# Optimization experiments

Hardware: AMD Instinct MI355X
Metric: run time of the kernel (lower is better)

The kernel has to match this reference:

```python
import jax, jax.numpy as jnp
import numpy as np

E = 65536          # number of edges (cell pairs)
D = 256            # hidden_dim
P = 8              # n_lr_pairs


def setup_inputs() -> dict:
    key = jax.random.key(0)
    k1, k2, k3, k4, k5, k6, k7 = jax.random.split(key, 7)
    scale = 1.0 / np.sqrt(D)
    z_src = jax.random.normal(k1, (E, D), dtype=jnp.float32)
    z_dst = jax.random.normal(k2, (E, D), dtype=jnp.float32)
    lr_pair_idx = jax.random.randint(k3, (E,), 0, P, dtype=jnp.int64)
    # Per-LR-pair Linear(D, D): y = x @ W.T + b  (torch convention, W: [out, in])
    W_lr = jax.random.normal(k4, (P, D, D), dtype=jnp.float32) * scale
    b_lr = jax.random.normal(k5, (P, D), dtype=jnp.float32) * scale
    # nn.Bilinear(D, D, 1): weight [1, D, D], bias [1]
    W_bil = jax.random.normal(k6, (1, D, D), dtype=jnp.float32) * scale
    b_bil = jax.random.normal(k7, (1,), dtype=jnp.float32) * scale
    return {"z_src": z_src, "z_dst": z_dst, "W_lr": W_lr, "b_lr": b_lr,
            "W_bil": W_bil, "b_bil": b_bil, "lr_pair_idx": lr_pair_idx}


def _forward(z_src, z_dst, W_lr, b_lr, W_bil, b_bil, lr_pair_idx):
    # Per-LR-pair linear projection of z_src (MoE-style routing).
    # Fixed small loop over P experts; each iteration is a dense GEMM over
    # all E edges, masked to the edges routed to that pair. All idx values
    # lie in [0, P), so the zeros-init in the original is fully overwritten.
    z_proj = jnp.zeros_like(z_src)
    for p in range(P):
        mask = (lr_pair_idx == p)[:, None]                      # [E, 1]
        y_p = z_src @ W_lr[p].T + b_lr[p]                       # [E, D]
        z_proj = jnp.where(mask, y_p, z_proj)
    # Bilinear scoring: score_e = z_proj_e @ W_bil[0] @ z_dst_e + b_bil
    t = z_proj @ W_bil[0]                                       # [E, D]
    scores = jnp.sum(t * z_dst, axis=-1, keepdims=True) + b_bil  # [E, 1]
    return scores


def reference(z_src, z_dst, W_lr, b_lr, W_bil, b_bil, lr_pair_idx):
    return _forward(z_src, z_dst, W_lr, b_lr, W_bil, b_bil, lr_pair_idx)
```

## Files before the change

kernel.cpp:

```cpp
#include <hip/hip_runtime.h>
#include <hip/hip_bf16.h>
#include <cstddef>

#define NE 65536
#define ND 256
#define NP 8
#define RBLK 64
#define EPB (NE / RBLK)
#define TR 32
#define MAXT 2056

typedef short bf16x8 __attribute__((ext_vector_type(8)));
typedef float f32x4  __attribute__((ext_vector_type(4)));

__device__ __forceinline__ unsigned short f2bf(float f) {
  unsigned int u = __float_as_uint(f);
  u += 0x7FFFu + ((u >> 16) & 1u);
  return (unsigned short)(u >> 16);
}
__device__ __forceinline__ float bf2f(unsigned short h) {
  return __uint_as_float(((unsigned int)h) << 16);
}
__device__ __forceinline__ int load_idx(const void* idxraw, int is32, int e) {
  return is32 ? ((const int*)idxraw)[e] : (int)((const long long*)idxraw)[e];
}
__device__ __forceinline__ int sniff_is32(const void* idxraw, int* lflag, int bsel) {
  int tid = threadIdx.x;
  if (tid == 0) *lflag = 0;
  __syncthreads();
  const unsigned int* w = (const unsigned int*)idxraw;
  unsigned int val = w[((bsel & 63) * 256 + tid) * 2 + 1];
  if (__any(val != 0) && (tid & 63) == 0) atomicOr(lflag, 1);
  __syncthreads();
  return *lflag;
}

__global__ __launch_bounds__(256) void k_pre0(const float* __restrict__ Wbil,
                                              const float* __restrict__ blr,
                                              const void* __restrict__ idxraw,
                                              unsigned short* __restrict__ WbT,
                                              float* __restrict__ v,
                                              int* __restrict__ counts) {
  int b = blockIdx.x, t = threadIdx.x;
  if (b < 32) {
    int s = b * 256 + t;
    int kt = s >> 10, c = (s >> 6) & 15, l = s & 63;
    int col = c * 16 + (l & 15);
    int k0 = kt * 32 + (l >> 4) * 8;
    union { uint4 u; unsigned short h[8]; } uu;
#pragma unroll
    for (int j = 0; j < 8; ++j)
      uu.h[j] = f2bf(Wbil[(k0 + j) * ND + col]);
    *(uint4*)(WbT + (size_t)s * 8) = uu.u;
  } else if (b < 40) {
    int p = b - 32;
    float s = 0.f;
    for (int k = 0; k < ND; ++k)
      s = fmaf(blr[p * ND + k], Wbil[k * ND + t], s);
    v[p * ND + t] = s;
  } else {
    __shared__ int h[NP];
    __shared__ int lflag;
    int hb = b - 40;
    int is32 = sniff_is32(idxraw, &lflag, hb);
    if (t < NP) h[t] = 0;
    __syncthreads();
    int base = hb * EPB;
#pragma unroll
    for (int i = 0; i < EPB / 256; ++i) {
      int p = load_idx(idxraw, is32, base + t + i * 256);
      atomicAdd(&h[p], 1);
    }
    __syncthreads();
    if (t < NP) counts[hb * NP + t] = h[t];
  }
}

__global__ __launch_bounds__(64) void k_scan(const int* __restrict__ counts,
                                             int* __restrict__ hdr,
                                             int* __restrict__ bases) {
  __shared__ int cnt[NP];
  __shared__ int off[NP + 1];
  int q = threadIdx.x;
  if (q < NP) {
    int s = 0;
    for (int b = 0; b < RBLK; ++b) s += counts[b * NP + q];
    cnt[q] = s;
  }
  __syncthreads();
  if (q == 0) {
    int o = 0, tt = 0;
    for (int p = 0; p < NP; ++p) {
      off[p] = o; hdr[p] = o; hdr[9 + p] = tt;
      o += cnt[p];
      tt += (cnt[p] + TR - 1) / TR;
    }
    off[NP] = o; hdr[NP] = o; hdr[9 + NP] = tt;
  }
  __syncthreads();
  if (q < NP) {
    int run = off[q];
    for (int b = 0; b < RBLK; ++b) {
      bases[b * NP + q] = run;
      run += counts[b * NP + q];
    }
  }
}

__global__ __launch_bounds__(256) void k_sc2(const void* __restrict__ idxraw,
                                             const int* __restrict__ bases,
                                             int* __restrict__ perm,
                                             const float* __restrict__ Wlr,
                                             const unsigned short* __restrict__ WbT,
                                             unsigned short* __restrict__ Cst) {
  __shared__ unsigned short aF[2048 * 8];
  int b = blockIdx.x, tid = threadIdx.x;
  if (b < 64) {
    __shared__ int cur[NP];
    __shared__ int lflag;
    int is32 = sniff_is32(idxraw, &lflag, b);
    if (tid < NP) cur[tid] = bases[b * NP + tid];
    __syncthreads();
    int base = b * EPB;
#pragma unroll
    for (int i = 0; i < EPB / 256; ++i) {
      int e = base + tid + i * 256;
      int p = load_idx(idxraw, is32, e);
      int slot = atomicAdd(&cur[p], 1);
      perm[slot] = e;
    }
    return;
  }
  int blk = b - 64;
  int p = blk >> 2;
  int i0 = (blk & 3) * 64;
  const float* Wp = Wlr + (size_t)p * ND * ND;
#pragma unroll
  for (int it = 0; it < 8; ++it) {
    int s = tid + it * 256;
    int kt = s >> 8, r = (s >> 6) & 3, l = s & 63;
    int i = r * 16 + (l & 15);
    int k0 = kt * 32 + (l >> 4) * 8;
    union { uint4 u; unsigned short h[8]; } uu;
#pragma unroll
    for (int j = 0; j < 8; ++j)
      uu.h[j] = f2bf(Wp[(size_t)(k0 + j) * ND + i0 + i]);
    *(uint4*)(aF + (size_t)s * 8) = uu.u;
  }
  __syncthreads();
  int w = tid >> 6, l = tid & 63;
  f32x4 zero = {0.f, 0.f, 0.f, 0.f};
  f32x4 acc[16];
#pragma unroll
  for (int c = 0; c < 16; ++c) acc[c] = zero;
  for (int kt = 0; kt < 8; ++kt) {
    bf16x8 a = *(const bf16x8*)(aF + (size_t)((kt * 4 + w) * 64 + l) * 8);
#pragma unroll
    for (int c = 0; c < 16; ++c) {
      bf16x8 bb = *(const bf16x8*)(WbT + (size_t)((kt * 16 + c) * 64 + l) * 8);
      acc[c] = __builtin_amdgcn_mfma_f32_16x16x32_bf16(a, bb, acc[c], 0, 0, 0);
    }
  }
  unsigned short* Cp = Cst + (size_t)p * ND * ND;
#pragma unroll
  for (int c = 0; c < 16; ++c) {
#pragma unroll
    for (int q = 0; q < 4; ++q) {
      int i = i0 + w * 16 + ((l >> 4) * 4) + q;
      int j = c * 16 + (l & 15);
      int pos = ((i >> 5) * 16 + (j >> 4)) * 512 + (((i >> 3) & 3) * 16 + (j & 15)) * 8 + (i & 7);
      Cp[pos] = f2bf(acc[c][q]);
    }
  }
}

__global__ __launch_bounds__(512, 8) void k_main(const float* __restrict__ zsrc,
                                                 const float* __restrict__ zdst,
                                                 const int* __restrict__ perm,
                                                 const int* __restrict__ hdr,
                                                 const unsigned short* __restrict__ Cst,
                                                 const float* __restrict__ v,
                                                 const float* __restrict__ bbil,
                                                 float* __restrict__ out) {
  __shared__ unsigned short zs[8192];
  __shared__ unsigned short zd[8192];
  __shared__ float red[8][TR];
  __shared__ int eids[TR];
  __shared__ int shdr[18];
  int tid = threadIdx.x;
  if (tid < 18) shdr[tid] = hdr[tid];
  __syncthreads();
  int bid = blockIdx.x;
  if (bid >= shdr[9 + NP]) return;
  int p = 0;
  while (p < NP - 1 && bid >= shdr[9 + p + 1]) ++p;
  int t = bid - shdr[9 + p];
  int cnt = shdr[p + 1] - shdr[p];
  int ebase = shdr[p] + t * TR;
  int nrow = cnt - t * TR; if (nrow > TR) nrow = TR;
  if (tid < TR) eids[tid] = perm[ebase + (tid < nrow ? tid : nrow - 1)];
  __syncthreads();
  int w = tid >> 6, l = tid & 63;
  int hh = l >> 4, rr = l & 15;

  int kt0 = l >> 3, q0 = (l >> 1) & 3, par0 = l & 1;
#pragma unroll
  for (int i = 0; i < 4; ++i) {
    int row = w * 4 + i;
    int e = eids[row];
    float4 fs = *(const float4*)(zsrc + (size_t)e * ND + l * 4);
    float4 fd = *(const float4*)(zdst + (size_t)e * ND + l * 4);
    union { unsigned long long u; unsigned short h[4]; } us, ud;
    us.h[0] = f2bf(fs.x); us.h[1] = f2bf(fs.y); us.h[2] = f2bf(fs.z); us.h[3] = f2bf(fs.w);
    ud.h[0] = f2bf(fd.x); ud.h[1] = f2bf(fd.y); ud.h[2] = f2bf(fd.z); ud.h[3] = f2bf(fd.w);
    unsigned g = (unsigned)((kt0 * 2 + (row >> 4)) * 64 + (row & 15) + 16 * q0);
    g ^= ((g >> 6) & 7u) << 1;
    *(unsigned long long*)((char*)zs + g * 16 + par0 * 8) = us.u;
    *(unsigned long long*)((char*)zd + ((unsigned)(row * 512 + l * 8) ^ (((unsigned)row & 7u) << 5))) = ud.u;
  }
  __syncthreads();

  const unsigned short* Cp = Cst + (size_t)p * ND * ND;
  f32x4 zero = {0.f, 0.f, 0.f, 0.f};
  f32x4 acc[2][2];
#pragma unroll
  for (int sr = 0; sr < 2; ++sr)
#pragma unroll
    for (int cl = 0; cl < 2; ++cl) acc[sr][cl] = zero;
#pragma unroll
  for (int kt = 0; kt < 8; ++kt) {
    bf16x8 a[2];
#pragma unroll
    for (int sr = 0; sr < 2; ++sr) {
      unsigned g = (unsigned)((kt * 2 + sr) * 64 + l);
      g ^= ((g >> 6) & 7u) << 1;
      a[sr] = *(const bf16x8*)((const char*)zs + g * 16);
    }
#pragma unroll
    for (int cl = 0; cl < 2; ++cl) {
      bf16x8 bb = *(const bf16x8*)(Cp + (size_t)((kt * 16 + (w * 2 + cl)) * 64 + l) * 8);
#pragma unroll
      for (int sr = 0; sr < 2; ++sr)
        acc[sr][cl] = __builtin_amdgcn_mfma_f32_16x16x32_bf16(a[sr], bb, acc[sr][cl], 0, 0, 0);
    }
  }

  float vloc[2];
#pragma unroll
  for (int cl = 0; cl < 2; ++cl)
    vloc[cl] = v[p * ND + (w * 2 + cl) * 16 + rr];
#pragma unroll
  for (int sr = 0; sr < 2; ++sr) {
#pragma unroll
    for (int q = 0; q < 4; ++q) {
      int row = sr * 16 + hh * 4 + q;
      unsigned swz = ((unsigned)row & 7u) << 5;
      float sv = 0.f;
#pragma unroll
      for (int cl = 0; cl < 2; ++cl) {
        int col = (w * 2 + cl) * 16 + rr;
        unsigned byte = ((unsigned)(row * 512 + col * 2)) ^ swz;
        sv = fmaf(acc[sr][cl][q] + vloc[cl], bf2f(*(const unsigned short*)((const char*)zd + byte)), sv);
      }
      sv += __shfl_xor(sv, 1, 64);
      sv += __shfl_xor(sv, 2, 64);
      sv += __shfl_xor(sv, 4, 64);
      sv += __shfl_xor(sv, 8, 64);
      if (rr == 0) red[w][row] = sv;
    }
  }
  __syncthreads();
  if (tid < TR && tid < nrow) {
    float sc = bbil[0];
#pragma unroll
    for (int ww = 0; ww < 8; ++ww) sc += red[ww][tid];
    out[eids[tid]] = sc;
  }
}

extern "C" void kernel_launch(void* const* d_in, const int* in_sizes, int n_in,
                              void* d_out, int out_size, void* d_ws, size_t ws_size,
                              hipStream_t stream) {
  const float* zsrc = (const float*)d_in[0];
  const float* zdst = (const float*)d_in[1];
  const float* Wlr  = (const float*)d_in[2];
  const float* blr  = (const float*)d_in[3];
  const float* Wbil = (const float*)d_in[4];
  const float* bbil = (const float*)d_in[5];
  const void*  idx  = (const void*)d_in[6];
  float* out = (float*)d_out;

  char* ws = (char*)d_ws;
  int* hdr    = (int*)ws;
  int* counts = (int*)(ws + 4096);
  int* bases  = (int*)(ws + 8192);
  int* perm   = (int*)(ws + 16384);
  unsigned short* WbT = (unsigned short*)(ws + 16384 + (size_t)NE * 4);
  float* v = (float*)(ws + 16384 + (size_t)NE * 4 + 131072);
  unsigned short* Cst = (unsigned short*)(ws + 16384 + (size_t)NE * 4 + 131072 + 8192);

  k_pre0<<<104, 256, 0, stream>>>(Wbil, blr, idx, WbT, v, counts);
  k_scan<<<1, 64, 0, stream>>>(counts, hdr, bases);
  k_sc2<<<96, 256, 0, stream>>>(idx, bases, perm, Wlr, WbT, Cst);
  k_main<<<MAXT, 512, 0, stream>>>(zsrc, zdst, perm, hdr, Cst, v, bbil, out);
}
```

Measured before the change: 77.90 us.

## Repack z_src/z_dst into expert-sorted bf16 buffers before the main GEMM

Adds a repack kernel that loads each 32-edge block of z_src/z_dst into LDS, computes per-expert ranks with wave ballots, and writes bf16 rows into permuted, expert-contiguous workspace buffers. The main kernel then reads those rows contiguously instead of gathering fp32 rows through perm. Counting is rewritten to use ballots over 32-edge sub-blocks, with a wider scan, and the scatter is split from the W_lr x W_bil precompute. This adds a full extra read and write pass over both inputs plus more launches, in exchange for coalesced, half-width loads in the main kernel. A gather fallback path runs when the workspace is too small.

After: 110.5 us. +41.9%, slower.

```diff
diff --git a/kernel.cpp b/kernel.cpp
--- a/kernel.cpp
+++ b/kernel.cpp
@@ -5,13 +5,15 @@
 #define NE 65536
 #define ND 256
 #define NP 8
-#define RBLK 64
-#define EPB (NE / RBLK)
+#define SB 32
+#define NSB (NE / SB)
 #define TR 32
 #define MAXT 2056
 
 typedef short bf16x8 __attribute__((ext_vector_type(8)));
 typedef float f32x4  __attribute__((ext_vector_type(4)));
+typedef const __attribute__((address_space(1))) unsigned int* gas_t;
+typedef __attribute__((address_space(3))) unsigned int* las_t;
 
 __device__ __forceinline__ unsigned short f2bf(float f) {
   unsigned int u = __float_as_uint(f);
@@ -24,12 +26,12 @@
 __device__ __forceinline__ int load_idx(const void* idxraw, int is32, int e) {
   return is32 ? ((const int*)idxraw)[e] : (int)((const long long*)idxraw)[e];
 }
-__device__ __forceinline__ int sniff_is32(const void* idxraw, int* lflag, int bsel) {
+__device__ __forceinline__ int sniff_is32(const void* idxraw, int* lflag) {
   int tid = threadIdx.x;
   if (tid == 0) *lflag = 0;
   __syncthreads();
   const unsigned int* w = (const unsigned int*)idxraw;
-  unsigned int val = w[((bsel & 63) * 256 + tid) * 2 + 1];
+  unsigned int val = w[(((int)blockIdx.x & 63) * 256 + (tid & 255)) * 2 + 1];
   if (__any(val != 0) && (tid & 63) == 0) atomicOr(lflag, 1);
   __syncthreads();
   return *lflag;
@@ -59,81 +61,64 @@
       s = fmaf(blr[p * ND + k], Wbil[k * ND + t], s);
     v[p * ND + t] = s;
   } else {
-    __shared__ int h[NP];
     __shared__ int lflag;
+    int is32 = sniff_is32(idxraw, &lflag);
     int hb = b - 40;
-    int is32 = sniff_is32(idxraw, &lflag, hb);
-    if (t < NP) h[t] = 0;
-    __syncthreads();
-    int base = hb * EPB;
-#pragma unroll
-    for (int i = 0; i < EPB / 256; ++i) {
-      int p = load_idx(idxraw, is32, base + t + i * 256);
-      atomicAdd(&h[p], 1);
-    }
-    __syncthreads();
-    if (t < NP) counts[hb * NP + t] = h[t];
-  }
-}
-
-__global__ __launch_bounds__(64) void k_scan(const int* __restrict__ counts,
-                                             int* __restrict__ hdr,
-                                             int* __restrict__ bases) {
-  __shared__ int cnt[NP];
-  __shared__ int off[NP + 1];
-  int q = threadIdx.x;
-  if (q < NP) {
-    int s = 0;
-    for (int b = 0; b < RBLK; ++b) s += counts[b * NP + q];
-    cnt[q] = s;
-  }
-  __syncthreads();
-  if (q == 0) {
+    int w = t >> 6, l = t & 63;
+    int e = hb * 256 + w * 64 + l;
+    int p = load_idx(idxraw, is32, e);
+    int sb0 = hb * 8 + w * 2;
+#pragma unroll
+    for (int q = 0; q < NP; ++q) {
+      unsigned long long m = __ballot(p == q);
+      if (l == q)      counts[q * NSB + sb0]     = __popcll(m & 0xFFFFFFFFull);
+      if (l == 32 + q) counts[q * NSB + sb0 + 1] = __popcll(m >> 32);
+    }
+  }
+}
+
+__global__ __launch_bounds__(256) void k_scan(const int* __restrict__ counts,
+                                              int* __restrict__ hdr,
+                                              int* __restrict__ bases) {
+  __shared__ int part[NP][32], cpre[NP][32], cnt[NP], shoff[NP];
+  int t = threadIdx.x;
+  int q = t >> 5, i = t & 31;
+  int s = 0;
+  for (int j = 0; j < 64; ++j) s += counts[q * NSB + i * 64 + j];
+  part[q][i] = s;
+  __syncthreads();
+  if (t < NP) {
+    int run = 0;
+    for (int k = 0; k < 32; ++k) { cpre[t][k] = run; run += part[t][k]; }
+    cnt[t] = run;
+  }
+  __syncthreads();
+  if (t == 0) {
     int o = 0, tt = 0;
     for (int p = 0; p < NP; ++p) {
-      off[p] = o; hdr[p] = o; hdr[9 + p] = tt;
+      shoff[p] = o; hdr[p] = o; hdr[9 + p] = tt;
       o += cnt[p];
       tt += (cnt[p] + TR - 1) / TR;
     }
-    off[NP] = o; hdr[NP] = o; hdr[9 + NP] = tt;
-  }
-  __syncthreads();
-  if (q < NP) {
-    int run = off[q];
-    for (int b = 0; b < RBLK; ++b) {
-      bases[b * NP + q] = run;
-      run += counts[b * NP + q];
-    }
-  }
-}
-
-__global__ __launch_bounds__(256) void k_sc2(const void* __restrict__ idxraw,
-                                             const int* __restrict__ bases,
-                                             int* __restrict__ perm,
-                                             const float* __restrict__ Wlr,
-                                             const unsigned short* __restrict__ WbT,
-                                             unsigned short* __restrict__ Cst) {
+    hdr[NP] = o; hdr[9 + NP] = tt;
+  }
+  __syncthreads();
+  int run = shoff[q] + cpre[q][i];
+  for (int j = 0; j < 64; ++j) {
+    int sb = i * 64 + j;
+    bases[q * NSB + sb] = run;
+    run += counts[q * NSB + sb];
+  }
+}
+
+__global__ __launch_bounds__(256) void k_cpre(const float* __restrict__ Wlr,
+                                              const unsigned short* __restrict__ WbT,
+                                              unsigned short* __restrict__ Cst) {
   __shared__ unsigned short aF[2048 * 8];
-  int b = blockIdx.x, tid = threadIdx.x;
-  if (b < 64) {
-    __shared__ int cur[NP];
-    __shared__ int lflag;
-    int is32 = sniff_is32(idxraw, &lflag, b);
-    if (tid < NP) cur[tid] = bases[b * NP + tid];
-    __syncthreads();
-    int base = b * EPB;
-#pragma unroll
-    for (int i = 0; i < EPB / 256; ++i) {
-      int e = base + tid + i * 256;
-      int p = load_idx(idxraw, is32, e);
-      int slot = atomicAdd(&cur[p], 1);
-      perm[slot] = e;
-    }
-    return;
-  }
-  int blk = b - 64;
+  int blk = blockIdx.x;
   int p = blk >> 2;
   int i0 = (blk & 3) * 64;
+  int tid = threadIdx.x;
   const float* Wp = Wlr + (size_t)p * ND * ND;
 #pragma unroll
   for (int it = 0; it < 8; ++it) {
@@ -174,14 +159,95 @@
   }
 }
 
-__global__ __launch_bounds__(512, 8) void k_main(const float* __restrict__ zsrc,
-                                                 const float* __restrict__ zdst,
-                                                 const int* __restrict__ perm,
-                                                 const int* __restrict__ hdr,
-                                                 const unsigned short* __restrict__ Cst,
-                                                 const float* __restrict__ v,
-                                                 const float* __restrict__ bbil,
-                                                 float* __restrict__ out) {
+__global__ __launch_bounds__(256) void k_repack(const void* __restrict__ idxraw,
+                                                const float* __restrict__ zsrc,
+                                                const float* __restrict__ zdst,
+                                                const int* __restrict__ bases,
+                                                int* __restrict__ perm,
+                                                unsigned short* __restrict__ zsP,
+                                                unsigned short* __restrict__ zdP) {
+  __shared__ float zsL[SB * 256];
+  __shared__ float zdL[SB * 256];
+  __shared__ int lsrcS[SB], garowS[SB];
+  __shared__ int lflag;
+  int tid = threadIdx.x;
+  int b = blockIdx.x;
+  int is32 = sniff_is32(idxraw, &lflag);
+  int w = tid >> 6, l = tid & 63;
+  int base = b * SB;
+#pragma unroll
+  for (int i = 0; i < 16; ++i) {
+    int r = w * 16 + i;
+    const float* g = (r < SB) ? (zsrc + (size_t)(base + r) * ND + l * 4)
+                              : (zdst + (size_t)(base + r - SB) * ND + l * 4);
+    float* ldsb = (r < SB) ? (zsL + r * 256) : (zdL + (r - SB) * 256);
+    __builtin_amdgcn_global_load_lds((gas_t)(const void*)g,
+                                     (las_t)(void*)ldsb, 16, 0, 0);
+  }
+  if (w == 0) {
+    int p = (l < SB) ? load_idx(idxraw, is32, base + l) : 999;
+    unsigned long long lt = (l == 63) ? ~0ull >> 1 : ((1ull << l) - 1ull);
+    int loffq = 0, slot = 0, rank = 0, gq = 0;
+#pragma unroll
+    for (int q = 0; q < NP; ++q) {
+      unsigned long long m = __ballot(p == q);
+      if (p == q) { rank = __popcll(m & lt); slot = loffq + rank; gq = q; }
+      loffq += __popcll(m);
+    }
+    if (l < SB) {
+      lsrcS[slot] = l;
+      int g = bases[gq * NSB + b] + rank;
+      garowS[slot] = g;
+      perm[g] = base + l;
+    }
+  }
+  __syncthreads();
+  int hw = tid >> 5, ln = tid & 31;
+#pragma unroll
+  for (int i = 0; i < 8; ++i) {
+    int orow = hw * 8 + i;
+    int s = orow & (SB - 1);
+    int n = lsrcS[s];
+    size_t g = (size_t)garowS[s];
+    const float* srcRow = (orow < SB) ? (zsL + n * 256) : (zdL + n * 256);
+    unsigned short* dst = ((orow < SB) ? zsP : zdP) + g * 256 + ln * 8;
+    float4 a0 = *(const float4*)(srcRow + ln * 8);
+    float4 a1 = *(const float4*)(srcRow + ln * 8 + 4);
+    union { uint4 u; unsigned short h[8]; } o;
+    o.h[0] = f2bf(a0.x); o.h[1] = f2bf(a0.y); o.h[2] = f2bf(a0.z); o.h[3] = f2bf(a0.w);
+    o.h[4] = f2bf(a1.x); o.h[5] = f2bf(a1.y); o.h[6] = f2bf(a1.z); o.h[7] = f2bf(a1.w);
+    *(uint4*)dst = o.u;
+  }
+}
+
+__global__ __launch_bounds__(64) void k_perm(const void* __restrict__ idxraw,
+                                             const int* __restrict__ bases,
+                                             int* __restrict__ perm) {
+  __shared__ int lflag;
+  int l = threadIdx.x;
+  int b = blockIdx.x;
+  int is32 = sniff_is32(idxraw, &lflag);
+  int base = b * SB;
+  int p = (l < SB) ? load_idx(idxraw, is32, base + l) : 999;
+  unsigned long long lt = (l == 63) ? ~0ull >> 1 : ((1ull << l) - 1ull);
+  int loffq = 0, rank = 0, gq = -1;
+#pragma unroll
+  for (int q = 0; q < NP; ++q) {
+    unsigned long long m = __ballot(p == q);
+    if (p == q) { rank = __popcll(m & lt); gq = q; }
+    loffq += __popcll(m);
+  }
+  if (l < SB) perm[bases[gq * NSB + b] + rank] = base + l;
+}
+
+__global__ __launch_bounds__(512, 8) void k_main_s(const unsigned short* __restrict__ zsP,
+                                                   const unsigned short* __restrict__ zdP,
+                                                   const int* __restrict__ perm,
+                                                   const int* __restrict__ hdr,
+                                                   const unsigned short* __restrict__ Cst,
+                                                   const float* __restrict__ v,
+                                                   const float* __restrict__ bbil,
+                                                   float* __restrict__ out) {
   __shared__ unsigned short zs[8192];
   __shared__ unsigned short zd[8192];
   __shared__ float red[8][TR];
@@ -199,10 +265,105 @@
   int ebase = shdr[p] + t * TR;
   int nrow = cnt - t * TR; if (nrow > TR) nrow = TR;
   if (tid < TR) eids[tid] = perm[ebase + (tid < nrow ? tid : nrow - 1)];
-  __syncthreads();
   int w = tid >> 6, l = tid & 63;
+  int kt0 = l >> 3, q0 = (l >> 1) & 3, par0 = l & 1;
+#pragma unroll
+  for (int i = 0; i < 4; ++i) {
+    int row = w * 4 + i;
+    int grow = ebase + row; if (grow > NE - 1) grow = NE - 1;
+    unsigned long long us = *(const unsigned long long*)(zsP + (size_t)grow * 256 + l * 4);
+    unsigned long long ud = *(const unsigned long long*)(zdP + (size_t)grow * 256 + l * 4);
+    unsigned g = (unsigned)((kt0 * 2 + (row >> 4)) * 64 + (row & 15) + 16 * q0);
+    g ^= ((g >> 6) & 7u) << 1;
+    *(unsigned long long*)((char*)zs + g * 16 + par0 * 8) = us;
+    *(unsigned long long*)((char*)zd + ((unsigned)(row * 512 + l * 8) ^ (((unsigned)row & 7u) << 5))) = ud;
+  }
+  __syncthreads();
+  const unsigned short* Cp = Cst + (size_t)p * ND * ND;
+  f32x4 zero = {0.f, 0.f, 0.f, 0.f};
+  f32x4 acc[2][2];
+#pragma unroll
+  for (int sr = 0; sr < 2; ++sr)
+#pragma unroll
+    for (int cl = 0; cl < 2; ++cl) acc[sr][cl] = zero;
   int hh = l >> 4, rr = l & 15;
-
+#pragma unroll
+  for (int kt = 0; kt < 8; ++kt) {
+    bf16x8 a[2];
+#pragma unroll
+    for (int sr = 0; sr < 2; ++sr) {
+      unsigned g = (unsigned)((kt * 2 + sr) * 64 + l);
+      g ^= ((g >> 6) & 7u) << 1;
+      a[sr] = *(const bf16x8*)((const char*)zs + g * 16);
+    }
+#pragma unroll
+    for (int cl = 0; cl < 2; ++cl) {
+      bf16x8 bb = *(const bf16x8*)(Cp + (size_t)((kt * 16 + (w * 2 + cl)) * 64 + l) * 8);
+#pragma unroll
+      for (int sr = 0; sr < 2; ++sr)
+        acc[sr][cl] = __builtin_amdgcn_mfma_f32_16x16x32_bf16(a[sr], bb, acc[sr][cl], 0, 0, 0);
+    }
+  }
+  float vloc[2];
+#pragma unroll
+  for (int cl = 0; cl < 2; ++cl)
+    vloc[cl] = v[p * ND + (w * 2 + cl) * 16 + rr];
+#pragma unroll
+  for (int sr = 0; sr < 2; ++sr) {
+#pragma unroll
+    for (int q = 0; q < 4; ++q) {
+      int row = sr * 16 + hh * 4 + q;
+      unsigned swz = ((unsigned)row & 7u) << 5;
+      float sv = 0.f;
+#pragma unroll
+      for (int cl = 0; cl < 2; ++cl) {
+        int col = (w * 2 + cl) * 16 + rr;
+        unsigned byte = ((unsigned)(row * 512 + col * 2)) ^ swz;
+        sv = fmaf(acc[sr][cl][q] + vloc[cl], bf2f(*(const unsigned short*)((const char*)zd + byte)), sv);
+      }
+      sv += __shfl_xor(sv, 1, 64);
+      sv += __shfl_xor(sv, 2, 64);
+      sv += __shfl_xor(sv, 4, 64);
+      sv += __shfl_xor(sv, 8, 64);
+      if (rr == 0) red[w][row] = sv;
+    }
+  }
+  __syncthreads();
+  if (tid < TR && tid < nrow) {
+    float sc = bbil[0];
+#pragma unroll
+    for (int ww = 0; ww < 8; ++ww) sc += red[ww][tid];
+    out[eids[tid]] = sc;
+  }
+}
+
+__global__ __launch_bounds__(512, 8) void k_main_g(const float* __restrict__ zsrc,
+                                                   const float* __restrict__ zdst,
+                                                   const int* __restrict__ perm,
+                                                   const int* __restrict__ hdr,
+                                                   const unsigned short* __restrict__ Cst,
+                                                   const float* __restrict__ v,
+                                                   const float* __restrict__ bbil,
+                                                   float* __restrict__ out) {
+  __shared__ unsigned short zs[8192];
+  __shared__ unsigned short zd[8192];
+  __shared__ float red[8][TR];
+  __shared__ int eids[TR];
+  __shared__ int shdr[18];
+  int tid = threadIdx.x;
+  if (tid < 18) shdr[tid] = hdr[tid];
+  __syncthreads();
+  int bid = blockIdx.x;
+  if (bid >= shdr[9 + NP]) return;
+  int p = 0;
+  while (p < NP - 1 && bid >= shdr[9 + p + 1]) ++p;
+  int t = bid - shdr[9 + p];
+  int cnt = shdr[p + 1] - shdr[p];
+  int ebase = shdr[p] + t * TR;
+  int nrow = cnt - t * TR; if (nrow > TR) nrow = TR;
+  if (tid < TR) eids[tid] = perm[ebase + (tid < nrow ? tid : nrow - 1)];
+  __syncthreads();
+  int w = tid >> 6, l = tid & 63;
   int kt0 = l >> 3, q0 = (l >> 1) & 3, par0 = l & 1;
 #pragma unroll
   for (int i = 0; i < 4; ++i) {
@@ -219,7 +380,6 @@
     *(unsigned long long*)((char*)zd + ((unsigned)(row * 512 + l * 8) ^ (((unsigned)row & 7u) << 5))) = ud.u;
   }
   __syncthreads();
-
   const unsigned short* Cp = Cst + (size_t)p * ND * ND;
   f32x4 zero = {0.f, 0.f, 0.f, 0.f};
   f32x4 acc[2][2];
@@ -227,6 +387,7 @@
   for (int sr = 0; sr < 2; ++sr)
 #pragma unroll
     for (int cl = 0; cl < 2; ++cl) acc[sr][cl] = zero;
+  int hh = l >> 4, rr = l & 15;
 #pragma unroll
   for (int kt = 0; kt < 8; ++kt) {
     bf16x8 a[2];
@@ -244,7 +405,6 @@
         acc[sr][cl] = __builtin_amdgcn_mfma_f32_16x16x32_bf16(a[sr], bb, acc[sr][cl], 0, 0, 0);
     }
   }
-
   float vloc[2];
 #pragma unroll
   for (int cl = 0; cl < 2; ++cl)
@@ -293,14 +453,23 @@
   char* ws = (char*)d_ws;
   int* hdr    = (int*)ws;
   int* counts = (int*)(ws + 4096);
-  int* bases  = (int*)(ws + 8192);
-  int* perm   = (int*)(ws + 16384);
-  unsigned short* WbT = (unsigned short*)(ws + 16384 + (size_t)NE * 4);
-  float* v = (float*)(ws + 16384 + (size_t)NE * 4 + 131072);
-  unsigned short* Cst = (unsigned short*)(ws + 16384 + (size_t)NE * 4 + 131072 + 8192);
-
-  k_pre0<<<104, 256, 0, stream>>>(Wbil, blr, idx, WbT, v, counts);
-  k_scan<<<1, 64, 0, stream>>>(counts, hdr, bases);
-  k_sc2<<<96, 256, 0, stream>>>(idx, bases, perm, Wlr, WbT, Cst);
-  k_main<<<MAXT, 512, 0, stream>>>(zsrc, zdst, perm, hdr, Cst, v, bbil, out);
-}
+  int* bases  = (int*)(ws + 73728);
+  unsigned short* WbT = (unsigned short*)(ws + 139264);
+  float* v            = (float*)(ws + 270336);
+  unsigned short* Cst = (unsigned short*)(ws + 278528);
+  int* perm           = (int*)(ws + 1327104);
+  unsigned short* zsP = (unsigned short*)(ws + 2097152);
+  unsigned short* zdP = (unsigned short*)(ws + 2097152 + 33554432);
+  size_t need = 2097152 + 2ull * 33554432;
+
+  k_pre0<<<296, 256, 0, stream>>>(Wbil, blr, idx, WbT, v, counts);
+  k_scan<<<1, 256, 0, stream>>>(counts, hdr, bases);
+  k_cpre<<<32, 256, 0, stream>>>(Wlr, WbT, Cst);
+  if (ws_size >= need) {
+    k_repack<<<NSB, 256, 0, stream>>>(idx, zsrc, zdst, bases, perm, zsP, zdP);
+    k_main_s<<<MAXT, 512, 0, stream>>>(zsP, zdP, perm, hdr, Cst, v, bbil, out);
+  } else {
+    k_perm<<<NSB, 64, 0, stream>>>(idx, bases, perm);
+    k_main_g<<<MAXT, 512, 0, stream>>>(zsrc, zdst, perm, hdr, Cst, v, bbil, out);
+  }
+}
```

## Make routing histogram and permutation deterministic via ballots and interleave expert tiles

Applied to the files above, without the earlier changes.

The per-block shared-memory atomic histogram and atomic scatter are replaced with wave ballot/popcount counts over 32-edge sub-blocks, a wider parallel scan, and a separate rank-based permutation kernel. Edges are now placed deterministically in order. The permutation scatter is split out of the fused weight-precompute kernel, adding one more launch. k_main now launches a fixed 16384-block grid with expert-interleaved block mapping, so tiles of different experts run at the same time, but many blocks exit early. The intent is to remove LDS atomic contention and the serial scan work, in exchange for extra launch overhead and idle blocks.

New measurement: 87.48 us. 12.3% more time.

```diff
diff --git a/kernel.cpp b/kernel.cpp
--- a/kernel.cpp
+++ b/kernel.cpp
@@ -5,10 +5,9 @@
 #define NE 65536
 #define ND 256
 #define NP 8
-#define RBLK 64
-#define EPB (NE / RBLK)
+#define SB 32
+#define NSB (NE / SB)
 #define TR 32
-#define MAXT 2056
 
 typedef short bf16x8 __attribute__((ext_vector_type(8)));
 typedef float f32x4  __attribute__((ext_vector_type(4)));
@@ -24,12 +23,12 @@
 __device__ __forceinline__ int load_idx(const void* idxraw, int is32, int e) {
   return is32 ? ((const int*)idxraw)[e] : (int)((const long long*)idxraw)[e];
 }
-__device__ __forceinline__ int sniff_is32(const void* idxraw, int* lflag, int bsel) {
+__device__ __forceinline__ int sniff_is32(const void* idxraw, int* lflag) {
   int tid = threadIdx.x;
   if (tid == 0) *lflag = 0;
   __syncthreads();
   const unsigned int* w = (const unsigned int*)idxraw;
-  unsigned int val = w[((bsel & 63) * 256 + tid) * 2 + 1];
+  unsigned int val = w[(((int)blockIdx.x & 63) * 256 + (tid & 255)) * 2 + 1];
   if (__any(val != 0) && (tid & 63) == 0) atomicOr(lflag, 1);
   __syncthreads();
   return *lflag;
@@ -59,81 +58,64 @@
       s = fmaf(blr[p * ND + k], Wbil[k * ND + t], s);
     v[p * ND + t] = s;
   } else {
-    __shared__ int h[NP];
     __shared__ int lflag;
+    int is32 = sniff_is32(idxraw, &lflag);
     int hb = b - 40;
-    int is32 = sniff_is32(idxraw, &lflag, hb);
-    if (t < NP) h[t] = 0;
-    __syncthreads();
-    int base = hb * EPB;
-#pragma unroll
-    for (int i = 0; i < EPB / 256; ++i) {
-      int p = load_idx(idxraw, is32, base + t + i * 256);
-      atomicAdd(&h[p], 1);
-    }
-    __syncthreads();
-    if (t < NP) counts[hb * NP + t] = h[t];
-  }
-}
-
-__global__ __launch_bounds__(64) void k_scan(const int* __restrict__ counts,
-                                             int* __restrict__ hdr,
-                                             int* __restrict__ bases) {
-  __shared__ int cnt[NP];
-  __shared__ int off[NP + 1];
-  int q = threadIdx.x;
-  if (q < NP) {
-    int s = 0;
-    for (int b = 0; b < RBLK; ++b) s += counts[b * NP + q];
-    cnt[q] = s;
-  }
-  __syncthreads();
-  if (q == 0) {
+    int w = t >> 6, l = t & 63;
+    int e = hb * 256 + w * 64 + l;
+    int p = load_idx(idxraw, is32, e);
+    int sb0 = hb * 8 + w * 2;
+#pragma unroll
+    for (int q = 0; q < NP; ++q) {
+      unsigned long long m = __ballot(p == q);
+      if (l == q)      counts[q * NSB + sb0]     = __popcll(m & 0xFFFFFFFFull);
+      if (l == 32 + q) counts[q * NSB + sb0 + 1] = __popcll(m >> 32);
+    }
+  }
+}
+
+__global__ __launch_bounds__(256) void k_scan(const int* __restrict__ counts,
+                                              int* __restrict__ hdr,
+                                              int* __restrict__ bases) {
+  __shared__ int part[NP][32], cpre[NP][32], cnt[NP], shoff[NP];
+  int t = threadIdx.x;
+  int q = t >> 5, i = t & 31;
+  int s = 0;
+  for (int j = 0; j < 64; ++j) s += counts[q * NSB + i * 64 + j];
+  part[q][i] = s;
+  __syncthreads();
+  if (t < NP) {
+    int run = 0;
+    for (int k = 0; k < 32; ++k) { cpre[t][k] = run; run += part[t][k]; }
+    cnt[t] = run;
+  }
+  __syncthreads();
+  if (t == 0) {
     int o = 0, tt = 0;
     for (int p = 0; p < NP; ++p) {
-      off[p] = o; hdr[p] = o; hdr[9 + p] = tt;
+      shoff[p] = o; hdr[p] = o; hdr[9 + p] = tt;
       o += cnt[p];
       tt += (cnt[p] + TR - 1) / TR;
     }
-    off[NP] = o; hdr[NP] = o; hdr[9 + NP] = tt;
-  }
-  __syncthreads();
-  if (q < NP) {
-    int run = off[q];
-    for (int b = 0; b < RBLK; ++b) {
-      bases[b * NP + q] = run;
-      run += counts[b * NP + q];
-    }
-  }
-}
-
-__global__ __launch_bounds__(256) void k_sc2(const void* __restrict__ idxraw,
-                                             const int* __restrict__ bases,
-                                             int* __restrict__ perm,
-                                             const float* __restrict__ Wlr,
-                                             const unsigned short* __restrict__ WbT,
-                                             unsigned short* __restrict__ Cst) {
+    hdr[NP] = o; hdr[9 + NP] = tt;
+  }
+  __syncthreads();
+  int run = shoff[q] + cpre[q][i];
+  for (int j = 0; j < 64; ++j) {
+    int sb = i * 64 + j;
+    bases[q * NSB + sb] = run;
+    run += counts[q * NSB + sb];
+  }
+}
+
+__global__ __launch_bounds__(256) void k_cpre(const float* __restrict__ Wlr,
+                                              const unsigned short* __restrict__ WbT,
+                                              unsigned short* __restrict__ Cst) {
   __shared__ unsigned short aF[2048 * 8];
-  int b = blockIdx.x, tid = threadIdx.x;
-  if (b < 64) {
-    __shared__ int cur[NP];
-    __shared__ int lflag;
-    int is32 = sniff_is32(idxraw, &lflag, b);
-    if (tid < NP) cur[tid] = bases[b * NP + tid];
-    __syncthreads();
-    int base = b * EPB;
-#pragma unroll
-    for (int i = 0; i < EPB / 256; ++i) {
-      int e = base + tid + i * 256;
-      int p = load_idx(idxraw, is32, e);
-      int slot = atomicAdd(&cur[p], 1);
-      perm[slot] = e;
-    }
-    return;
-  }
-  int blk = b - 64;
+  int blk = blockIdx.x;
   int p = blk >> 2;
   int i0 = (blk & 3) * 64;
+  int tid = threadIdx.x;
   const float* Wp = Wlr + (size_t)p * ND * ND;
 #pragma unroll
   for (int it = 0; it < 8; ++it) {
@@ -172,6 +154,33 @@
       Cp[pos] = f2bf(acc[c][q]);
     }
   }
+}
+
+__global__ __launch_bounds__(64) void k_perm(const void* __restrict__ idxraw,
+                                             const int* __restrict__ bases,
+                                             int* __restrict__ perm) {
+  __shared__ int lflag;
+  int l = threadIdx.x;
+  int b = blockIdx.x;
+  if (l == 0) lflag = 0;
+  __syncthreads();
+  {
+    const unsigned int* w = (const unsigned int*)idxraw;
+    unsigned int val = w[((b & 63) * 64 + l) * 2 + 1];
+    if (__any(val != 0) && l == 0) atomicOr(&lflag, 1);
+  }
+  __syncthreads();
+  int is32 = lflag;
+  int base = b * SB;
+  int p = (l < SB) ? load_idx(idxraw, is32, base + l) : 999;
+  unsigned long long lt = (l == 63) ? (~0ull >> 1) : ((1ull << l) - 1ull);
+  int rank = 0, gq = 0;
+#pragma unroll
+  for (int q = 0; q < NP; ++q) {
+    unsigned long long m = __ballot(p == q);
+    if (p == q) { rank = __popcll(m & lt); gq = q; }
+  }
+  if (l < SB) perm[bases[gq * NSB + b] + rank] = base + l;
 }
 
 __global__ __launch_bounds__(512, 8) void k_main(const float* __restrict__ zsrc,
@@ -191,18 +200,16 @@
   if (tid < 18) shdr[tid] = hdr[tid];
   __syncthreads();
   int bid = blockIdx.x;
-  if (bid >= shdr[9 + NP]) return;
-  int p = 0;
-  while (p < NP - 1 && bid >= shdr[9 + p + 1]) ++p;
-  int t = bid - shdr[9 + p];
+  int g = bid >> 3, r = bid & 7;
+  int p = g & 7;
+  int t = ((g >> 3) << 3) + r;
   int cnt = shdr[p + 1] - shdr[p];
+  if (t * TR >= cnt) return;
   int ebase = shdr[p] + t * TR;
   int nrow = cnt - t * TR; if (nrow > TR) nrow = TR;
   if (tid < TR) eids[tid] = perm[ebase + (tid < nrow ? tid : nrow - 1)];
   __syncthreads();
   int w = tid >> 6, l = tid & 63;
-  int hh = l >> 4, rr = l & 15;
-
   int kt0 = l >> 3, q0 = (l >> 1) & 3, par0 = l & 1;
 #pragma unroll
   for (int i = 0; i < 4; ++i) {
@@ -213,13 +220,12 @@
     union { unsigned long long u; unsigned short h[4]; } us, ud;
     us.h[0] = f2bf(fs.x); us.h[1] = f2bf(fs.y); us.h[2] = f2bf(fs.z); us.h[3] = f2bf(fs.w);
     ud.h[0] = f2bf(fd.x); ud.h[1] = f2bf(fd.y); ud.h[2] = f2bf(fd.z); ud.h[3] = f2bf(fd.w);
-    unsigned g = (unsigned)((kt0 * 2 + (row >> 4)) * 64 + (row & 15) + 16 * q0);
-    g ^= ((g >> 6) & 7u) << 1;
-    *(unsigned long long*)((char*)zs + g * 16 + par0 * 8) = us.u;
+    unsigned gg = (unsigned)((kt0 * 2 + (row >> 4)) * 64 + (row & 15) + 16 * q0);
+    gg ^= ((gg >> 6) & 7u) << 1;
+    *(unsigned long long*)((char*)zs + gg * 16 + par0 * 8) = us.u;
     *(unsigned long long*)((char*)zd + ((unsigned)(row * 512 + l * 8) ^ (((unsigned)row & 7u) << 5))) = ud.u;
   }
   __syncthreads();
-
   const unsigned short* Cp = Cst + (size_t)p * ND * ND;
   f32x4 zero = {0.f, 0.f, 0.f, 0.f};
   f32x4 acc[2][2];
@@ -227,14 +233,15 @@
   for (int sr = 0; sr < 2; ++sr)
 #pragma unroll
     for (int cl = 0; cl < 2; ++cl) acc[sr][cl] = zero;
+  int hh = l >> 4, rr = l & 15;
 #pragma unroll
   for (int kt = 0; kt < 8; ++kt) {
     bf16x8 a[2];
 #pragma unroll
     for (int sr = 0; sr < 2; ++sr) {
-      unsigned g = (unsigned)((kt * 2 + sr) * 64 + l);
-      g ^= ((g >> 6) & 7u) << 1;
-      a[sr] = *(const bf16x8*)((const char*)zs + g * 16);
+      unsigned gg = (unsigned)((kt * 2 + sr) * 64 + l);
+      gg ^= ((gg >> 6) & 7u) << 1;
+      a[sr] = *(const bf16x8*)((const char*)zs + gg * 16);
     }
 #pragma unroll
     for (int cl = 0; cl < 2; ++cl) {
@@ -244,7 +251,6 @@
         acc[sr][cl] = __builtin_amdgcn_mfma_f32_16x16x32_bf16(a[sr], bb, acc[sr][cl], 0, 0, 0);
     }
   }
-
   float vloc[2];
 #pragma unroll
   for (int cl = 0; cl < 2; ++cl)
@@ -293,14 +299,15 @@
   char* ws = (char*)d_ws;
   int* hdr    = (int*)ws;
   int* counts = (int*)(ws + 4096);
-  int* bases  = (int*)(ws + 8192);
-  int* perm   = (int*)(ws + 16384);
-  unsigned short* WbT = (unsigned short*)(ws + 16384 + (size_t)NE * 4);
-  float* v = (float*)(ws + 16384 + (size_t)NE * 4 + 131072);
-  unsigned short* Cst = (unsigned short*)(ws + 16384 + (size_t)NE * 4 + 131072 + 8192);
-
-  k_pre0<<<104, 256, 0, stream>>>(Wbil, blr, idx, WbT, v, counts);
-  k_scan<<<1, 64, 0, stream>>>(counts, hdr, bases);
-  k_sc2<<<96, 256, 0, stream>>>(idx, bases, perm, Wlr, WbT, Cst);
-  k_main<<<MAXT, 512, 0, stream>>>(zsrc, zdst, perm, hdr, Cst, v, bbil, out);
-}
+  int* bases  = (int*)(ws + 73728);
+  unsigned short* WbT = (unsigned short*)(ws + 139264);
+  float* v            = (float*)(ws + 270336);
+  unsigned short* Cst = (unsigned short*)(ws + 278528);
+  int* perm           = (int*)(ws + 1327104);
+
+  k_pre0<<<296, 256, 0, stream>>>(Wbil, blr, idx, WbT, v, counts);
+  k_scan<<<1, 256, 0, stream>>>(counts, hdr, bases);
+  k_cpre<<<32, 256, 0, stream>>>(Wlr, WbT, Cst);
+  k_perm<<<NSB, 64, 0, stream>>>(idx, bases, perm);
+  k_main<<<16384, 512, 0, stream>>>(zsrc, zdst, perm, hdr, Cst, v, bbil, out);
+}
```
